# Kernel tuning notes

Measured on AMD Instinct MI355X. Metric: run time of the kernel, lower is better.

Reference implementation:

```python
import jax, jax.numpy as jnp
from jax import lax
import numpy as np

B, C_IN, C_OUT, H, MODES, L = 16, 128, 128, 8, 256, 16384
HEAD_IN, HEAD_OUT = C_IN // H, C_OUT // H


def setup_inputs() -> dict:
    key = jax.random.key(0)
    ks = jax.random.split(key, 6)
    init_std = (2.0 / (C_IN + C_OUT)) ** 0.5
    return {
        "x": jax.random.normal(ks[0], (B, C_IN, L), dtype=jnp.float32),
        "weight_re": init_std * jax.random.normal(ks[1], (H, HEAD_IN, HEAD_OUT, MODES), dtype=jnp.float32),
        "weight_im": init_std * jax.random.normal(ks[2], (H, HEAD_IN, HEAD_OUT, MODES), dtype=jnp.float32),
        "bias": init_std * jax.random.normal(ks[3], (C_OUT, 1), dtype=jnp.float32),
        "conv_w": (1.0 / np.sqrt(C_IN * 3)) * jax.random.normal(ks[4], (C_OUT, C_IN, 3), dtype=jnp.float32),
        "conv_b": (1.0 / np.sqrt(C_IN * 3)) * jax.random.normal(ks[5], (C_OUT,), dtype=jnp.float32),
        "gate": jnp.array(0.0, dtype=jnp.float32),
    }


def reference(x, weight_re, weight_im, bias, conv_w, conv_b, gate):
    b, _, n = x.shape
    # rfft with norm='forward' (forward transform scaled by 1/n)
    x_freq = jnp.fft.rfft(x, axis=-1, norm="forward")            # (b, C_IN, n//2+1) complex
    x_freq = x_freq.reshape(b, H, HEAD_IN, -1)                    # (b, h, i, f)
    w = weight_re + 1j * weight_im                                # (h, i, o, MODES)
    # truncated low-frequency complex mixing per head
    out_freq = jnp.einsum("bhif,hiof->bhof", x_freq[..., :MODES], w)
    out_freq = out_freq.reshape(b, C_OUT, MODES)
    # irfft zero-pads the truncated spectrum back to n//2+1 modes
    x_out = jnp.fft.irfft(out_freq, n=n, axis=-1, norm="forward")  # (b, C_OUT, n) real
    x_out = x_out + bias                                           # bias: (C_OUT, 1)
    # local conv branch: Conv1d(kernel=3, padding=1) == SAME
    local = lax.conv_general_dilated(
        x, conv_w, window_strides=(1,), padding="SAME",
        dimension_numbers=("NCH", "OIH", "NCH"),
    ) + conv_b[None, :, None]
    g = jax.nn.sigmoid(gate)
    return g * x_out + (1.0 - g) * local
```

## Files before the change

### kernel.cpp

```cpp
#include <hip/hip_runtime.h>


typedef __bf16 bf16x8 __attribute__((ext_vector_type(8)));
typedef __bf16 bf16x4 __attribute__((ext_vector_type(4)));
typedef float f32x4 __attribute__((ext_vector_type(4)));
typedef unsigned short ushort8v __attribute__((ext_vector_type(8)));

#define PI2_OVER_L 3.8349519697141029073e-4f

#define GLD16(gp, lp) __builtin_amdgcn_global_load_lds( \
    (const __attribute__((address_space(1))) void*)(gp), \
    (__attribute__((address_space(3))) void*)(lp), 16, 0, 0)


__global__ void gen_kern(__bf16* __restrict__ Fjt, __bf16* __restrict__ Gtj,
                         const float* __restrict__ cw, __bf16* __restrict__ wbf,
                         const float* __restrict__ gate, int fold) {
    unsigned bid = blockIdx.x;
    if (bid < 16384u) {
        unsigned idx = bid * 256u + threadIdx.x;
        unsigned k = idx >> 14, t = idx & 16383u;
        unsigned m = (k * t) & 16383u;
        float th = (float)m * PI2_OVER_L;
        float s, c;
        __sincosf(th, &s, &c);
        const float inv = 1.0f / 16384.0f;
        Fjt[((size_t)(2u * k) << 14) + t]      = (__bf16)(c * inv);
        Fjt[((size_t)(2u * k + 1u) << 14) + t] = (__bf16)(-s * inv);
    } else if (bid < 32768u) {
        unsigned idx = (bid - 16384u) * 256u + threadIdx.x;
        unsigned t = idx >> 8, k = idx & 255u;
        unsigned m = (k * t) & 16383u;
        float th = (float)m * PI2_OVER_L;
        float s, c;
        __sincosf(th, &s, &c);
        float a = (k == 0u) ? 1.0f : 2.0f;
        if (fold) a *= 1.0f / (1.0f + __expf(-gate[0]));
        size_t base = ((size_t)t << 9) + 2u * k;
        Gtj[base]     = (__bf16)(a * c);
        Gtj[base + 1] = (__bf16)(-a * s);
    } else {
        int idx = (int)(bid - 32768u) * 256 + threadIdx.x;
        float sc = 1.0f;
        if (fold) sc = 1.0f - 1.0f / (1.0f + __expf(-gate[0]));
        int co = idx / 384, r = idx - co * 384, ci = r / 3, d = r - ci * 3;
        wbf[d * 16384 + co * 128 + ci] = (__bf16)(cw[idx] * sc);
    }
}

__global__ __launch_bounds__(256) void xpose_kern(const float* __restrict__ x,
        __bf16* __restrict__ xb, __bf16* __restrict__ xTb, int write_xb) {
    __shared__ __align__(16) __bf16 tile[128 * 64];
    int bid = blockIdx.x;
    int b = bid >> 8, tB = bid & 255, t0 = tB << 6;
    int tid = threadIdx.x;
    for (int idx = tid; idx < 2048; idx += 256) {
        int ci = idx >> 4, ch = idx & 15;
        size_t gp = ((size_t)((b << 7) + ci) << 14) + t0 + (ch << 2);
        float4 v = *(const float4*)(x + gp);
        bf16x4 p;
        p[0] = (__bf16)v.x; p[1] = (__bf16)v.y; p[2] = (__bf16)v.z; p[3] = (__bf16)v.w;
        *(bf16x4*)((char*)tile + (ci << 7) + (((ch >> 1) ^ ((ci >> 3) & 7)) << 4) + ((ch & 1) << 3)) = p;
        if (write_xb) *(bf16x4*)(xb + gp) = p;
    }
    __syncthreads();
    for (int idx = tid; idx < 1024; idx += 256) {
        int t = idx >> 4, ch = idx & 15;
        bf16x8 v;
#pragma unroll
        for (int j = 0; j < 8; j++) {
            int ci = (ch << 3) + j;
            v[j] = *(const __bf16*)((char*)tile + (ci << 7) +
                     ((((t >> 3) ^ ((ci >> 3) & 7))) << 4) + ((t & 7) << 1));
        }
        *(bf16x8*)(xTb + (((size_t)(b << 14)) + t0 + t) * 128 + ch * 8) = v;
    }
}

template<int ABF>
__global__ __launch_bounds__(256) void fwd_kern(const float* __restrict__ xf,
        const __bf16* __restrict__ xbv, const __bf16* __restrict__ Fjt,
        float* __restrict__ Cp, int kchunk) {
    __shared__ __align__(16) char smem[32768];
    int bid = blockIdx.x;
    int mt = bid & 15, nt = (bid >> 4) & 3, ks = bid >> 6;
    int tid = threadIdx.x, lane = tid & 63, wv = tid >> 6;
    int wm = (wv >> 1) << 6, wn = (wv & 1) << 6, lm = lane & 15;
    int rx = lm & 7;
    int r8 = lane >> 3, c8 = lane & 7;
    int srcoff = (c8 ^ r8) << 3;
    int ldrow = (wv << 5) + r8;
    char* ldst = smem + (wv << 12);
    f32x4 acc[4][4] = {};
    int k0 = ks * kchunk;
    const __bf16* ag = xbv + (((size_t)(mt * 128 + ldrow)) << 14) + k0 + srcoff;
    const __bf16* bg = Fjt + (((size_t)(nt * 128 + ldrow)) << 14) + k0 + srcoff;
    int frow = tid >> 1;
    const float* agf = xf + (((size_t)(mt * 128 + frow)) << 14) + k0;
    for (int kk = 0; kk < kchunk; kk += 64) {
        if (ABF) {
#pragma unroll
            for (int q = 0; q < 4; q++)
                GLD16(ag + (((size_t)q) << 17) + kk, ldst + (q << 10));
        } else {
#pragma unroll
            for (int q = 0; q < 4; q++) {
                int sl = ((tid & 1) << 2) + q;
                const float4* p = (const float4*)(agf + kk + (sl << 3));
                float4 v0 = p[0], v1 = p[1];
                bf16x8 t;
                t[0] = (__bf16)v0.x; t[1] = (__bf16)v0.y; t[2] = (__bf16)v0.z; t[3] = (__bf16)v0.w;
                t[4] = (__bf16)v1.x; t[5] = (__bf16)v1.y; t[6] = (__bf16)v1.z; t[7] = (__bf16)v1.w;
                *(bf16x8*)(smem + (frow << 7) + ((sl ^ (frow & 7)) << 4)) = t;
            }
        }
#pragma unroll
        for (int q = 0; q < 4; q++)
            GLD16(bg + (((size_t)q) << 17) + kk, ldst + 16384 + (q << 10));
        __syncthreads();
#pragma unroll
        for (int ks2 = 0; ks2 < 64; ks2 += 32) {
            int wb = (ks2 >> 3) + (lane >> 4);
            int wa = (wb ^ rx) << 4;
            bf16x8 af[4], bfv[4];
#pragma unroll
            for (int i = 0; i < 4; i++)
                af[i] = *(const bf16x8*)(smem + ((wm + i * 16 + lm) << 7) + wa);
#pragma unroll
            for (int j = 0; j < 4; j++)
                bfv[j] = *(const bf16x8*)(smem + 16384 + ((wn + j * 16 + lm) << 7) + wa);
#pragma unroll
            for (int i = 0; i < 4; i++)
#pragma unroll
                for (int j = 0; j < 4; j++)
                    acc[i][j] = __builtin_amdgcn_mfma_f32_16x16x32_bf16(af[i], bfv[j], acc[i][j], 0, 0, 0);
        }
        __syncthreads();
    }
    float* outp = Cp + (size_t)ks * (2048 * 512);
    int q = lane >> 4, cl = lane & 15;
#pragma unroll
    for (int i = 0; i < 4; i++)
#pragma unroll
        for (int j = 0; j < 4; j++) {
            int col = nt * 128 + wn + j * 16 + cl;
#pragma unroll
            for (int r = 0; r < 4; r++) {
                int row = mt * 128 + wm + i * 16 + q * 4 + r;
                outp[(size_t)row * 512 + col] = acc[i][j][r];
            }
        }
}

__global__ __launch_bounds__(256) void mix_kern(const float* __restrict__ Cp,
        const float* __restrict__ wre, const float* __restrict__ wim,
        __bf16* __restrict__ Ob, int ns) {
    __shared__ __align__(16) float Fs[16 * 256];
    int bid = blockIdx.x, bh = bid >> 1, kh = bid & 1;
    int b = bh >> 3, h = bh & 7;
    int tid = threadIdx.x;
    size_t base = (size_t)(b * 128 + h * 16) * 512 + kh * 256;
    for (int idx = tid; idx < 1024; idx += 256) {
        int i = idx >> 6, jj = (idx & 63) << 2;
        const float* p = Cp + base + (size_t)i * 512 + jj;
        f32x4 v = {};
#pragma unroll 4
        for (int s = 0; s < ns; s++) v += *(const f32x4*)(p + (size_t)s * 1048576);
        *(f32x4*)&Fs[i * 256 + jj] = v;
    }
    __syncthreads();
    for (int idx = tid; idx < 2048; idx += 256) {
        int o = idx >> 7, kl = idx & 127;
        int k = kh * 128 + kl;
        float ar = 0.f, ai = 0.f;
        const float* wr0 = wre + ((size_t)(h * 256 + o) << 8) + k;
        const float* wi0 = wim + ((size_t)(h * 256 + o) << 8) + k;
#pragma unroll 4
        for (int i = 0; i < 16; i++) {
            float fr = Fs[i * 256 + 2 * kl], fi = Fs[i * 256 + 2 * kl + 1];
            float wr = wr0[(size_t)i * 4096], wi = wi0[(size_t)i * 4096];
            ar += fr * wr - fi * wi;
            ai += fr * wi + fi * wr;
        }
        size_t ro = (size_t)(b * 128 + h * 16 + o) * 512;
        Ob[ro + 2 * k]     = (__bf16)ar;
        Ob[ro + 2 * k + 1] = (__bf16)ai;
    }
}

__global__ __launch_bounds__(256) void fused_kern(const __bf16* __restrict__ Ob,
        const __bf16* __restrict__ Gtj, const __bf16* __restrict__ wbf,
        const __bf16* __restrict__ xTb, const float* __restrict__ bias,
        const float* __restrict__ cb, const float* __restrict__ gate,
        float* __restrict__ out) {
    __shared__ __align__(16) char smem[33024];
    int bid = blockIdx.x, b = bid & 15, tt = bid >> 4;
    int t0 = tt << 7;
    int tid = threadIdx.x, lane = tid & 63, wv = tid >> 6;
    int wm = (wv >> 1) << 6, wn = (wv & 1) << 6, lm = lane & 15;
    int rx = lm & 7;
    int r8 = lane >> 3, c8 = lane & 7;
    int srcoff = (c8 ^ r8) << 3;
    int ldrow = (wv << 5) + r8;
    char* ldst = smem + (wv << 12);
    f32x4 acc[4][4] = {};

    {
        const __bf16* ag = Ob  + ((size_t)(b  * 128 + ldrow) << 9) + srcoff;
        const __bf16* bg = Gtj + ((size_t)(tt * 128 + ldrow) << 9) + srcoff;
        for (int k0 = 0; k0 < 512; k0 += 64) {
#pragma unroll
            for (int q = 0; q < 4; q++) {
                GLD16(ag + ((size_t)q << 12) + k0, ldst + (q << 10));
                GLD16(bg + ((size_t)q << 12) + k0, ldst + 16384 + (q << 10));
            }
            __syncthreads();
#pragma unroll
            for (int ks2 = 0; ks2 < 64; ks2 += 32) {
                int wb = (ks2 >> 3) + (lane >> 4);
                int wa = (wb ^ rx) << 4;
                bf16x8 af[4], bfv[4];
#pragma unroll
                for (int i = 0; i < 4; i++)
                    af[i] = *(const bf16x8*)(smem + ((wm + i * 16 + lm) << 7) + wa);
#pragma unroll
                for (int j = 0; j < 4; j++)
                    bfv[j] = *(const bf16x8*)(smem + 16384 + ((wn + j * 16 + lm) << 7) + wa);
#pragma unroll
                for (int i = 0; i < 4; i++)
#pragma unroll
                    for (int j = 0; j < 4; j++)
                        acc[i][j] = __builtin_amdgcn_mfma_f32_16x16x32_bf16(af[i], bfv[j], acc[i][j], 0, 0, 0);
            }
            __syncthreads();
        }
    }

    {
        char* xT = smem + 16384;
        for (int c0p = 0; c0p < 2; c0p++) {
            int c0 = c0p << 6;
            if (c0p) __syncthreads();
            for (int idx = tid; idx < 1040; idx += 256) {
                int row = idx >> 3, ch = idx & 7;
                int tg = t0 - 1 + row;
                ushort8v v = {};
                if (tg >= 0 && tg < 16384)
                    v = *(const ushort8v*)(xTb + ((((size_t)(b << 14)) + tg) << 7) + c0 + (ch << 3));
                *(ushort8v*)(xT + (row << 7) + ((ch ^ (row & 7)) << 4)) = v;
            }
            const __bf16* wg = wbf + (ldrow << 7) + c0 + srcoff;
            for (int d = 0; d < 3; d++) {
                if (d) __syncthreads();
#pragma unroll
                for (int q = 0; q < 4; q++)
                    GLD16(wg + d * 16384 + (q << 10), ldst + (q << 10));
                __syncthreads();
#pragma unroll
                for (int ks2 = 0; ks2 < 64; ks2 += 32) {
                    int wb = (ks2 >> 3) + (lane >> 4);
                    int wa = (wb ^ rx) << 4;
                    bf16x8 af[4], bfv[4];
#pragma unroll
                    for (int i = 0; i < 4; i++)
                        af[i] = *(const bf16x8*)(smem + ((wm + i * 16 + lm) << 7) + wa);
#pragma unroll
                    for (int j = 0; j < 4; j++) {
                        int r2 = wn + j * 16 + lm + d;
                        bfv[j] = *(const bf16x8*)(xT + (r2 << 7) + ((wb ^ (r2 & 7)) << 4));
                    }
#pragma unroll
                    for (int i = 0; i < 4; i++)
#pragma unroll
                        for (int j = 0; j < 4; j++)
                            acc[i][j] = __builtin_amdgcn_mfma_f32_16x16x32_bf16(af[i], bfv[j], acc[i][j], 0, 0, 0);
                }
            }
        }
    }

    float g = 1.0f / (1.0f + __expf(-gate[0]));
    int q = lane >> 4, cl = lane & 15;
#pragma unroll
    for (int i = 0; i < 4; i++)
#pragma unroll
        for (int j = 0; j < 4; j++) {
            int t = t0 + wn + j * 16 + cl;
#pragma unroll
            for (int r = 0; r < 4; r++) {
                int co = wm + i * 16 + q * 4 + r;
                float gb = g * bias[co] + (1.0f - g) * cb[co];
                out[((size_t)(b * 128 + co) << 14) + t] = acc[i][j][r] + gb;
            }
        }
}

#define SA 72
#define SXC 40
__global__ __launch_bounds__(256) void conv_kern(const float* __restrict__ x,
        const __bf16* __restrict__ wbf, const float* __restrict__ cb,
        float* __restrict__ out) {
    __shared__ __align__(16) __bf16 xT[130 * SXC];
    __shared__ __align__(16) __bf16 wS[3 * 128 * SXC];
    int bid = blockIdx.x, b = bid >> 7, t0 = (bid & 127) << 7;
    int tid = threadIdx.x, lane = tid & 63, wv = tid >> 6;
    int wm = (wv >> 1) << 6, wn = (wv & 1) << 6;
    f32x4 acc[4][4] = {};
    for (int c0 = 0; c0 < 128; c0 += 32) {
        for (int idx = tid; idx < 1536; idx += 256) {
            int d = idx / 512, rem = idx - d * 512, co = rem >> 2, g = rem & 3;
            ushort8v v = *(const ushort8v*)(wbf + d * 16384 + co * 128 + c0 + g * 8);
            *(ushort8v*)&wS[d * (128 * SXC) + co * SXC + g * 8] = v;
        }
        for (int idx = tid; idx < 4160; idx += 256) {
            int cc = idx / 130, tl = idx - cc * 130;
            int tg = t0 + tl - 1;
            float v = 0.f;
            if (tg >= 0 && tg < 16384)
                v = x[((size_t)(b * 128 + c0 + cc) << 14) + tg];
            xT[tl * SXC + cc] = (__bf16)v;
        }
        __syncthreads();
        int kf = (lane >> 4) << 3;
#pragma unroll
        for (int d = 0; d < 3; d++) {
            bf16x8 af[4], bfv[4];
#pragma unroll
            for (int i = 0; i < 4; i++)
                af[i] = *(const bf16x8*)&wS[d * (128 * SXC) + (wm + i * 16 + (lane & 15)) * SXC + kf];
#pragma unroll
            for (int j = 0; j < 4; j++)
                bfv[j] = *(const bf16x8*)&xT[(wn + j * 16 + (lane & 15) + d) * SXC + kf];
#pragma unroll
            for (int i = 0; i < 4; i++)
#pragma unroll
                for (int j = 0; j < 4; j++)
                    acc[i][j] = __builtin_amdgcn_mfma_f32_16x16x32_bf16(af[i], bfv[j], acc[i][j], 0, 0, 0);
        }
        __syncthreads();
    }
    int q = lane >> 4, cl = lane & 15;
#pragma unroll
    for (int i = 0; i < 4; i++)
#pragma unroll
        for (int j = 0; j < 4; j++) {
            int t = t0 + wn + j * 16 + cl;
#pragma unroll
            for (int r = 0; r < 4; r++) {
                int co = wm + i * 16 + q * 4 + r;
                out[((size_t)(b * 128 + co) << 14) + t] = acc[i][j][r] + cb[co];
            }
        }
}

__global__ __launch_bounds__(256) void inv_kern(const __bf16* __restrict__ Ob,
        const __bf16* __restrict__ Gtj, const float* __restrict__ bias,
        const float* __restrict__ gate, float* __restrict__ out) {
    __shared__ __align__(16) __bf16 As[128 * SA];
    __shared__ __align__(16) __bf16 Bs[128 * SA];
    int bid = blockIdx.x, mt = bid & 15, tt = bid >> 4;
    int tid = threadIdx.x, lane = tid & 63, wv = tid >> 6;
    int wm = (wv >> 1) << 6, wn = (wv & 1) << 6;
    f32x4 acc[4][4] = {};
    int arow = tid >> 1, ahalf = (tid & 1) << 5;
    const __bf16* ag = Ob  + (size_t)(mt * 128 + arow) * 512 + ahalf;
    const __bf16* bg = Gtj + (size_t)(tt * 128 + arow) * 512 + ahalf;
    __bf16* ad = &As[arow * SA + ahalf];
    __bf16* bd = &Bs[arow * SA + ahalf];
    for (int k0 = 0; k0 < 512; k0 += 64) {
#pragma unroll
        for (int q = 0; q < 4; q++) {
            ((ushort8v*)ad)[q] = ((const ushort8v*)(ag + k0))[q];
            ((ushort8v*)bd)[q] = ((const ushort8v*)(bg + k0))[q];
        }
        __syncthreads();
#pragma unroll
        for (int ks2 = 0; ks2 < 64; ks2 += 32) {
            int kf = ks2 + ((lane >> 4) << 3);
            bf16x8 af[4], bfv[4];
#pragma unroll
            for (int i = 0; i < 4; i++)
                af[i] = *(const bf16x8*)&As[(wm + i * 16 + (lane & 15)) * SA + kf];
#pragma unroll
            for (int j = 0; j < 4; j++)
                bfv[j] = *(const bf16x8*)&Bs[(wn + j * 16 + (lane & 15)) * SA + kf];
#pragma unroll
            for (int i = 0; i < 4; i++)
#pragma unroll
                for (int j = 0; j < 4; j++)
                    acc[i][j] = __builtin_amdgcn_mfma_f32_16x16x32_bf16(af[i], bfv[j], acc[i][j], 0, 0, 0);
        }
        __syncthreads();
    }
    float g = 1.0f / (1.0f + __expf(-gate[0]));
    float gi = 1.0f - g;
    int q = lane >> 4, cl = lane & 15;
#pragma unroll
    for (int i = 0; i < 4; i++)
#pragma unroll
        for (int j = 0; j < 4; j++) {
            int col = (tt << 7) + wn + j * 16 + cl;
#pragma unroll
            for (int r = 0; r < 4; r++) {
                int row = mt * 128 + wm + i * 16 + q * 4 + r;
                size_t oi = ((size_t)row << 14) + col;
                out[oi] = g * (acc[i][j][r] + bias[row & 127]) + gi * out[oi];
            }
        }
}

extern "C" void kernel_launch(void* const* d_in, const int* in_sizes, int n_in,
                              void* d_out, int out_size, void* d_ws, size_t ws_size,
                              hipStream_t stream) {
    const float* x    = (const float*)d_in[0];
    const float* wre  = (const float*)d_in[1];
    const float* wim  = (const float*)d_in[2];
    const float* bias = (const float*)d_in[3];
    const float* cw   = (const float*)d_in[4];
    const float* cb   = (const float*)d_in[5];
    const float* gate = (const float*)d_in[6];
    float* out = (float*)d_out;
    char* ws = (char*)d_ws;

    const size_t SZ_F = 16777216, SZ_G = 16777216, SZ_W = 98304;
    const size_t SZ_X = 67108864, SZ_CP8 = 33554432, SZ_CP4 = 16777216, SZ_OB = 2097152;
    size_t oG = SZ_F, oW = oG + SZ_G, oEnd = oW + SZ_W;

    size_t needT3 = oEnd + 2 * SZ_X + SZ_CP8 + SZ_OB;
    size_t needT2 = oEnd + SZ_X + SZ_CP8 + SZ_OB;
    size_t needT1 = oEnd + SZ_X + SZ_CP4 + SZ_OB;

    __bf16* Fjt = (__bf16*)(ws);
    __bf16* Gtj = (__bf16*)(ws + oG);
    __bf16* wbf = (__bf16*)(ws + oW);

    if (ws_size >= needT1) {
        int use_xb = (ws_size >= needT3);
        int ns = (ws_size >= needT2) ? 8 : 4;
        __bf16* xb  = use_xb ? (__bf16*)(ws + oEnd) : nullptr;
        __bf16* xTb = (__bf16*)(ws + oEnd + (use_xb ? SZ_X : 0));
        float*  Cp  = (float*)((char*)xTb + SZ_X);
        __bf16* Ob  = (__bf16*)((char*)Cp + (size_t)ns * 4194304);
        int kchunk = 16384 / ns;

        gen_kern<<<32960, 256, 0, stream>>>(Fjt, Gtj, cw, wbf, gate, 1);
        xpose_kern<<<4096, 256, 0, stream>>>(x, xb, xTb, use_xb);
        if (use_xb)
            fwd_kern<1><<<64 * ns, 256, 0, stream>>>(x, xb, Fjt, Cp, kchunk);
        else
            fwd_kern<0><<<64 * ns, 256, 0, stream>>>(x, nullptr, Fjt, Cp, kchunk);
        mix_kern<<<256, 256, 0, stream>>>(Cp, wre, wim, Ob, ns);
        fused_kern<<<2048, 256, 0, stream>>>(Ob, Gtj, wbf, xTb, bias, cb, gate, out);
    } else {
        float*  Cp  = (float*)(ws + oEnd);
        size_t need8 = oEnd + 8ull * 4194304ull + SZ_OB;
        int ns = (ws_size >= need8) ? 8 : 4;
        __bf16* Ob  = (__bf16*)(ws + oEnd + (size_t)ns * 4194304);
        int kchunk = 16384 / ns;

        gen_kern<<<32960, 256, 0, stream>>>(Fjt, Gtj, cw, wbf, gate, 0);
        fwd_kern<0><<<64 * ns, 256, 0, stream>>>(x, nullptr, Fjt, Cp, kchunk);
        mix_kern<<<256, 256, 0, stream>>>(Cp, wre, wim, Ob, ns);
        conv_kern<<<2048, 256, 0, stream>>>(x, wbf, cb, out);
        inv_kern<<<2048, 256, 0, stream>>>(Ob, Gtj, bias, gate, out);
    }
}
```

Baseline: 458.5 us.

## Double-buffer LDS in forward DFT and fused inverse/conv GEMM kernels

Switches fwd_kern and fused_kern to dynamic shared memory with two A/B LDS buffers, so the next K tile's global_load_lds is issued while MFMAs run on the current one. The conv stage now loads the transposed x tile by direct-to-LDS copies plus a small edge fix-up, instead of a thread loop, and it is chained into the same ping-pong pipeline. fwd_kern also reorders its block index so that consecutive blocks share the same M/N tile across K splits, for better L2 reuse. The cost is doubled LDS use (64-65KB per block), which lowers occupancy.

```diff
diff --git a/kernel.cpp b/kernel.cpp
--- a/kernel.cpp
+++ b/kernel.cpp
@@ -81,28 +81,67 @@
 __global__ __launch_bounds__(256) void fwd_kern(const float* __restrict__ xf,
         const __bf16* __restrict__ xbv, const __bf16* __restrict__ Fjt,
         float* __restrict__ Cp, int kchunk) {
-    __shared__ __align__(16) char smem[32768];
+    extern __shared__ __align__(16) char smem[];
     int bid = blockIdx.x;
-    int mt = bid & 15, nt = (bid >> 4) & 3, ks = bid >> 6;
+    int ks, mt, nt;
+    if (kchunk == 2048) { ks = bid & 7; nt = (bid >> 3) & 3; mt = bid >> 5; }
+    else               { ks = bid & 3; nt = (bid >> 2) & 3; mt = bid >> 4; }
     int tid = threadIdx.x, lane = tid & 63, wv = tid >> 6;
     int wm = (wv >> 1) << 6, wn = (wv & 1) << 6, lm = lane & 15;
     int rx = lm & 7;
     int r8 = lane >> 3, c8 = lane & 7;
     int srcoff = (c8 ^ r8) << 3;
     int ldrow = (wv << 5) + r8;
-    char* ldst = smem + (wv << 12);
     f32x4 acc[4][4] = {};
     int k0 = ks * kchunk;
     const __bf16* ag = xbv + (((size_t)(mt * 128 + ldrow)) << 14) + k0 + srcoff;
     const __bf16* bg = Fjt + (((size_t)(nt * 128 + ldrow)) << 14) + k0 + srcoff;
-    int frow = tid >> 1;
-    const float* agf = xf + (((size_t)(mt * 128 + frow)) << 14) + k0;
-    for (int kk = 0; kk < kchunk; kk += 64) {
-        if (ABF) {
-#pragma unroll
-            for (int q = 0; q < 4; q++)
-                GLD16(ag + (((size_t)q) << 17) + kk, ldst + (q << 10));
-        } else {
+
+    char* A0 = smem;          char* B0 = smem + 16384;
+    char* A1 = smem + 32768;  char* B1 = smem + 49152;
+
+    auto COMPUTE = [&](const char* A, const char* B) {
+#pragma unroll
+        for (int ks2 = 0; ks2 < 64; ks2 += 32) {
+            int wb = (ks2 >> 3) + (lane >> 4);
+            int wa = (wb ^ rx) << 4;
+            bf16x8 af[4], bfv[4];
+#pragma unroll
+            for (int i = 0; i < 4; i++)
+                af[i] = *(const bf16x8*)(A + ((wm + i * 16 + lm) << 7) + wa);
+#pragma unroll
+            for (int j = 0; j < 4; j++)
+                bfv[j] = *(const bf16x8*)(B + ((wn + j * 16 + lm) << 7) + wa);
+#pragma unroll
+            for (int i = 0; i < 4; i++)
+#pragma unroll
+                for (int j = 0; j < 4; j++)
+                    acc[i][j] = __builtin_amdgcn_mfma_f32_16x16x32_bf16(af[i], bfv[j], acc[i][j], 0, 0, 0);
+        }
+    };
+
+    if (ABF) {
+        auto STAGE = [&](char* A, char* B, int kk) {
+#pragma unroll
+            for (int q = 0; q < 4; q++) {
+                GLD16(ag + (((size_t)q) << 17) + kk, A + (wv << 12) + (q << 10));
+                GLD16(bg + (((size_t)q) << 17) + kk, B + (wv << 12) + (q << 10));
+            }
+        };
+        STAGE(A0, B0, 0);
+        __syncthreads();
+        for (int kk = 0; kk < kchunk; kk += 128) {
+            STAGE(A1, B1, kk + 64);
+            COMPUTE(A0, B0);
+            __syncthreads();
+            if (kk + 128 < kchunk) STAGE(A0, B0, kk + 128);
+            COMPUTE(A1, B1);
+            __syncthreads();
+        }
+    } else {
+        int frow = tid >> 1;
+        const float* agf = xf + (((size_t)(mt * 128 + frow)) << 14) + k0;
+        for (int kk = 0; kk < kchunk; kk += 64) {
 #pragma unroll
             for (int q = 0; q < 4; q++) {
                 int sl = ((tid & 1) << 2) + q;
@@ -111,32 +150,17 @@
                 bf16x8 t;
                 t[0] = (__bf16)v0.x; t[1] = (__bf16)v0.y; t[2] = (__bf16)v0.z; t[3] = (__bf16)v0.w;
                 t[4] = (__bf16)v1.x; t[5] = (__bf16)v1.y; t[6] = (__bf16)v1.z; t[7] = (__bf16)v1.w;
-                *(bf16x8*)(smem + (frow << 7) + ((sl ^ (frow & 7)) << 4)) = t;
-            }
-        }
-#pragma unroll
-        for (int q = 0; q < 4; q++)
-            GLD16(bg + (((size_t)q) << 17) + kk, ldst + 16384 + (q << 10));
-        __syncthreads();
-#pragma unroll
-        for (int ks2 = 0; ks2 < 64; ks2 += 32) {
-            int wb = (ks2 >> 3) + (lane >> 4);
-            int wa = (wb ^ rx) << 4;
-            bf16x8 af[4], bfv[4];
-#pragma unroll
-            for (int i = 0; i < 4; i++)
-                af[i] = *(const bf16x8*)(smem + ((wm + i * 16 + lm) << 7) + wa);
-#pragma unroll
-            for (int j = 0; j < 4; j++)
-                bfv[j] = *(const bf16x8*)(smem + 16384 + ((wn + j * 16 + lm) << 7) + wa);
-#pragma unroll
-            for (int i = 0; i < 4; i++)
-#pragma unroll
-                for (int j = 0; j < 4; j++)
-                    acc[i][j] = __builtin_amdgcn_mfma_f32_16x16x32_bf16(af[i], bfv[j], acc[i][j], 0, 0, 0);
-        }
-        __syncthreads();
-    }
+                *(bf16x8*)(A0 + (frow << 7) + ((sl ^ (frow & 7)) << 4)) = t;
+            }
+#pragma unroll
+            for (int q = 0; q < 4; q++)
+                GLD16(bg + (((size_t)q) << 17) + kk, B0 + (wv << 12) + (q << 10));
+            __syncthreads();
+            COMPUTE(A0, B0);
+            __syncthreads();
+        }
+    }
+
     float* outp = Cp + (size_t)ks * (2048 * 512);
     int q = lane >> 4, cl = lane & 15;
 #pragma unroll
@@ -193,7 +217,7 @@
         const __bf16* __restrict__ xTb, const float* __restrict__ bias,
         const float* __restrict__ cb, const float* __restrict__ gate,
         float* __restrict__ out) {
-    __shared__ __align__(16) char smem[33024];
+    extern __shared__ __align__(16) char smem[];
     int bid = blockIdx.x, b = bid & 15, tt = bid >> 4;
     int t0 = tt << 7;
     int tid = threadIdx.x, lane = tid & 63, wv = tid >> 6;
@@ -202,82 +226,116 @@
     int r8 = lane >> 3, c8 = lane & 7;
     int srcoff = (c8 ^ r8) << 3;
     int ldrow = (wv << 5) + r8;
-    char* ldst = smem + (wv << 12);
     f32x4 acc[4][4] = {};
 
-    {
-        const __bf16* ag = Ob  + ((size_t)(b  * 128 + ldrow) << 9) + srcoff;
-        const __bf16* bg = Gtj + ((size_t)(tt * 128 + ldrow) << 9) + srcoff;
-        for (int k0 = 0; k0 < 512; k0 += 64) {
-#pragma unroll
-            for (int q = 0; q < 4; q++) {
-                GLD16(ag + ((size_t)q << 12) + k0, ldst + (q << 10));
-                GLD16(bg + ((size_t)q << 12) + k0, ldst + 16384 + (q << 10));
-            }
-            __syncthreads();
-#pragma unroll
-            for (int ks2 = 0; ks2 < 64; ks2 += 32) {
-                int wb = (ks2 >> 3) + (lane >> 4);
-                int wa = (wb ^ rx) << 4;
-                bf16x8 af[4], bfv[4];
-#pragma unroll
-                for (int i = 0; i < 4; i++)
-                    af[i] = *(const bf16x8*)(smem + ((wm + i * 16 + lm) << 7) + wa);
+    char* A0 = smem;          char* B0 = smem + 16640;
+    char* A1 = smem + 33280;  char* B1 = smem + 49920;
+
+    const __bf16* ag = Ob  + ((size_t)(b  * 128 + ldrow) << 9) + srcoff;
+    const __bf16* bg = Gtj + ((size_t)(tt * 128 + ldrow) << 9) + srcoff;
+    const __bf16* wg = wbf + (ldrow << 7) + srcoff;
+    const __bf16* xg = xTb + ((((size_t)(b << 14)) + t0 + (wv << 5) + r8) << 7)
+                           + ((c8 ^ ((1 + r8) & 7)) << 3);
+
+    auto STAGE_AB = [&](char* A, char* B, int kk) {
+#pragma unroll
+        for (int q = 0; q < 4; q++) {
+            GLD16(ag + ((size_t)q << 12) + kk, A + (wv << 12) + (q << 10));
+            GLD16(bg + ((size_t)q << 12) + kk, B + (wv << 12) + (q << 10));
+        }
+    };
+    auto STAGE_W = [&](char* A, int d, int c0) {
+#pragma unroll
+        for (int q = 0; q < 4; q++)
+            GLD16(wg + d * 16384 + c0 + (q << 10), A + (wv << 12) + (q << 10));
+    };
+    auto STAGE_X = [&](char* X, int c0) {
+#pragma unroll
+        for (int q = 0; q < 4; q++)
+            GLD16(xg + c0 + (q << 10), X + 128 + (wv << 12) + (q << 10));
+    };
+    auto EDGE_X = [&](char* X, int c0) {
+        if (tid < 16) {
+            int rr = (tid >> 3) ? 129 : 0;
+            int ch = tid & 7;
+            int tg = t0 - 1 + rr;
+            ushort8v v = {};
+            if (tg >= 0 && tg < 16384)
+                v = *(const ushort8v*)(xTb + (((size_t)(b << 14)) + tg) * 128 + c0 + ch * 8);
+            *(ushort8v*)(X + (rr << 7) + ((ch ^ (rr & 7)) << 4)) = v;
+        }
+    };
+    auto SPECC = [&](const char* A, const char* B) {
+#pragma unroll
+        for (int ks2 = 0; ks2 < 64; ks2 += 32) {
+            int wb = (ks2 >> 3) + (lane >> 4);
+            int wa = (wb ^ rx) << 4;
+            bf16x8 af[4], bfv[4];
+#pragma unroll
+            for (int i = 0; i < 4; i++)
+                af[i] = *(const bf16x8*)(A + ((wm + i * 16 + lm) << 7) + wa);
+#pragma unroll
+            for (int j = 0; j < 4; j++)
+                bfv[j] = *(const bf16x8*)(B + ((wn + j * 16 + lm) << 7) + wa);
+#pragma unroll
+            for (int i = 0; i < 4; i++)
 #pragma unroll
                 for (int j = 0; j < 4; j++)
-                    bfv[j] = *(const bf16x8*)(smem + 16384 + ((wn + j * 16 + lm) << 7) + wa);
-#pragma unroll
-                for (int i = 0; i < 4; i++)
-#pragma unroll
-                    for (int j = 0; j < 4; j++)
-                        acc[i][j] = __builtin_amdgcn_mfma_f32_16x16x32_bf16(af[i], bfv[j], acc[i][j], 0, 0, 0);
-            }
-            __syncthreads();
-        }
-    }
-
-    {
-        char* xT = smem + 16384;
-        for (int c0p = 0; c0p < 2; c0p++) {
-            int c0 = c0p << 6;
-            if (c0p) __syncthreads();
-            for (int idx = tid; idx < 1040; idx += 256) {
-                int row = idx >> 3, ch = idx & 7;
-                int tg = t0 - 1 + row;
-                ushort8v v = {};
-                if (tg >= 0 && tg < 16384)
-                    v = *(const ushort8v*)(xTb + ((((size_t)(b << 14)) + tg) << 7) + c0 + (ch << 3));
-                *(ushort8v*)(xT + (row << 7) + ((ch ^ (row & 7)) << 4)) = v;
-            }
-            const __bf16* wg = wbf + (ldrow << 7) + c0 + srcoff;
-            for (int d = 0; d < 3; d++) {
-                if (d) __syncthreads();
-#pragma unroll
-                for (int q = 0; q < 4; q++)
-                    GLD16(wg + d * 16384 + (q << 10), ldst + (q << 10));
-                __syncthreads();
-#pragma unroll
-                for (int ks2 = 0; ks2 < 64; ks2 += 32) {
-                    int wb = (ks2 >> 3) + (lane >> 4);
-                    int wa = (wb ^ rx) << 4;
-                    bf16x8 af[4], bfv[4];
-#pragma unroll
-                    for (int i = 0; i < 4; i++)
-                        af[i] = *(const bf16x8*)(smem + ((wm + i * 16 + lm) << 7) + wa);
-#pragma unroll
-                    for (int j = 0; j < 4; j++) {
-                        int r2 = wn + j * 16 + lm + d;
-                        bfv[j] = *(const bf16x8*)(xT + (r2 << 7) + ((wb ^ (r2 & 7)) << 4));
-                    }
-#pragma unroll
-                    for (int i = 0; i < 4; i++)
-#pragma unroll
-                        for (int j = 0; j < 4; j++)
-                            acc[i][j] = __builtin_amdgcn_mfma_f32_16x16x32_bf16(af[i], bfv[j], acc[i][j], 0, 0, 0);
-                }
-            }
-        }
-    }
+                    acc[i][j] = __builtin_amdgcn_mfma_f32_16x16x32_bf16(af[i], bfv[j], acc[i][j], 0, 0, 0);
+        }
+    };
+    auto CONVC = [&](const char* A, const char* X, int d) {
+#pragma unroll
+        for (int ks2 = 0; ks2 < 64; ks2 += 32) {
+            int wb = (ks2 >> 3) + (lane >> 4);
+            int wa = (wb ^ rx) << 4;
+            bf16x8 af[4], bfv[4];
+#pragma unroll
+            for (int i = 0; i < 4; i++)
+                af[i] = *(const bf16x8*)(A + ((wm + i * 16 + lm) << 7) + wa);
+#pragma unroll
+            for (int j = 0; j < 4; j++) {
+                int r2 = wn + j * 16 + lm + d;
+                bfv[j] = *(const bf16x8*)(X + (r2 << 7) + ((wb ^ (r2 & 7)) << 4));
+            }
+#pragma unroll
+            for (int i = 0; i < 4; i++)
+#pragma unroll
+                for (int j = 0; j < 4; j++)
+                    acc[i][j] = __builtin_amdgcn_mfma_f32_16x16x32_bf16(af[i], bfv[j], acc[i][j], 0, 0, 0);
+        }
+    };
+
+    STAGE_AB(A0, B0, 0);
+    __syncthreads();
+#pragma unroll
+    for (int kp = 0; kp < 4; kp++) {
+        int k0 = kp * 128;
+        STAGE_AB(A1, B1, k0 + 64);
+        SPECC(A0, B0);
+        __syncthreads();
+        if (kp < 3) {
+            STAGE_AB(A0, B0, k0 + 128);
+        } else {
+            STAGE_W(A0, 0, 0);
+            STAGE_X(B0, 0);
+            EDGE_X(B0, 0);
+        }
+        SPECC(A1, B1);
+        __syncthreads();
+    }
+
+    CONVC(A0, B0, 0);  STAGE_W(A1, 1, 0);  STAGE_X(B1, 64);  EDGE_X(B1, 64);
+    __syncthreads();
+    CONVC(A1, B0, 1);  STAGE_W(A0, 2, 0);
+    __syncthreads();
+    CONVC(A0, B0, 2);  STAGE_W(A1, 0, 64);
+    __syncthreads();
+    CONVC(A1, B1, 0);  STAGE_W(A0, 1, 64);
+    __syncthreads();
+    CONVC(A0, B1, 1);  STAGE_W(A1, 2, 64);
+    __syncthreads();
+    CONVC(A1, B1, 2);
 
     float g = 1.0f / (1.0f + __expf(-gate[0]));
     int q = lane >> 4, cl = lane & 15;
@@ -446,11 +504,11 @@
         gen_kern<<<32960, 256, 0, stream>>>(Fjt, Gtj, cw, wbf, gate, 1);
         xpose_kern<<<4096, 256, 0, stream>>>(x, xb, xTb, use_xb);
         if (use_xb)
-            fwd_kern<1><<<64 * ns, 256, 0, stream>>>(x, xb, Fjt, Cp, kchunk);
+            fwd_kern<1><<<64 * ns, 256, 65536, stream>>>(x, xb, Fjt, Cp, kchunk);
         else
-            fwd_kern<0><<<64 * ns, 256, 0, stream>>>(x, nullptr, Fjt, Cp, kchunk);
+            fwd_kern<0><<<64 * ns, 256, 32768, stream>>>(x, nullptr, Fjt, Cp, kchunk);
         mix_kern<<<256, 256, 0, stream>>>(Cp, wre, wim, Ob, ns);
-        fused_kern<<<2048, 256, 0, stream>>>(Ob, Gtj, wbf, xTb, bias, cb, gate, out);
+        fused_kern<<<2048, 256, 66560, stream>>>(Ob, Gtj, wbf, xTb, bias, cb, gate, out);
     } else {
         float*  Cp  = (float*)(ws + oEnd);
         size_t need8 = oEnd + 8ull * 4194304ull + SZ_OB;
@@ -459,7 +517,7 @@
         int kchunk = 16384 / ns;
 
         gen_kern<<<32960, 256, 0, stream>>>(Fjt, Gtj, cw, wbf, gate, 0);
-        fwd_kern<0><<<64 * ns, 256, 0, stream>>>(x, nullptr, Fjt, Cp, kchunk);
+        fwd_kern<0><<<64 * ns, 256, 32768, stream>>>(x, nullptr, Fjt, Cp, kchunk);
         mix_kern<<<256, 256, 0, stream>>>(Cp, wre, wim, Ob, ns);
         conv_kern<<<2048, 256, 0, stream>>>(x, wbf, cb, out);
         inv_kern<<<2048, 256, 0, stream>>>(Ob, Gtj, bias, gate, out);
```

Measured after the change: 427.8 us. 1.07x faster.
